# Kernel tuning notes

Hardware: AMD Instinct MI355X
Metric: run time of the kernel (lower is better)

## Reference

```python
import jax, jax.numpy as jnp
import numpy as np

N_NODES = 50000
EPS_BN = 1e-5

def _gat_layer(x, W, a_src, a_dst, b, src, dst):
    # PyG GATConv: h = xW per head; e = LeakyReLU(a_src.h_j + a_dst.h_i);
    # softmax over incoming edges per destination; out_i = sum alpha_e * h_j.
    N = x.shape[0]
    H, C = a_src.shape
    h = (x @ W).reshape(N, H, C)                       # [N,H,C]
    s = jnp.sum(h * a_src[None], axis=-1)              # [N,H] source term
    d = jnp.sum(h * a_dst[None], axis=-1)              # [N,H] dest term
    e = jax.nn.leaky_relu(s[src] + d[dst], 0.2)        # [E,H]
    m = jax.ops.segment_max(e, dst, num_segments=N)
    m = jnp.where(jnp.isfinite(m), m, 0.0)             # isolated nodes
    ex = jnp.exp(e - m[dst])                           # [E,H]
    denom = jax.ops.segment_sum(ex, dst, num_segments=N)
    alpha = ex / (denom[dst] + 1e-16)                  # [E,H]
    out = jax.ops.segment_sum(alpha[:, :, None] * h[src], dst, num_segments=N)
    return out.reshape(N, H * C) + b

def _bn_eval(x, gamma, beta, mean, var):
    return (x - mean) * jax.lax.rsqrt(var + EPS_BN) * gamma + beta

def setup_inputs() -> dict:
    key = jax.random.key(0)
    ks = jax.random.split(key, 12)
    N, E, Fin, H = N_NODES, 800000, 128, 4
    C1, C2 = 64, 32
    x = jax.random.normal(ks[0], (N, Fin), jnp.float32)
    edge_index = jax.random.randint(ks[1], (2, E), 0, N, jnp.int64)
    sc = lambda f: 1.0 / np.sqrt(f)
    return {
        "x": x, "edge_index": edge_index,
        "W1": jax.random.normal(ks[2], (Fin, H * C1), jnp.float32) * sc(Fin),
        "a1_src": jax.random.normal(ks[3], (H, C1), jnp.float32) * sc(C1),
        "a1_dst": jax.random.normal(ks[4], (H, C1), jnp.float32) * sc(C1),
        "b1": jnp.zeros((H * C1,), jnp.float32),
        "g1": jnp.ones((H * C1,), jnp.float32),
        "be1": jnp.zeros((H * C1,), jnp.float32),
        "m1": jnp.zeros((H * C1,), jnp.float32),
        "v1": jnp.ones((H * C1,), jnp.float32),
        "W2": jax.random.normal(ks[5], (H * C1, H * C2), jnp.float32) * sc(H * C1),
        "a2_src": jax.random.normal(ks[6], (H, C2), jnp.float32) * sc(C2),
        "a2_dst": jax.random.normal(ks[7], (H, C2), jnp.float32) * sc(C2),
        "b2": jnp.zeros((H * C2,), jnp.float32),
        "g2": jnp.ones((H * C2,), jnp.float32),
        "be2": jnp.zeros((H * C2,), jnp.float32),
        "m2": jnp.zeros((H * C2,), jnp.float32),
        "v2": jnp.ones((H * C2,), jnp.float32),
        "fcW": jax.random.normal(ks[8], (H * C2, 1), jnp.float32) * sc(H * C2),
        "fcb": jnp.zeros((1,), jnp.float32),
    }

def reference(x, edge_index, W1, a1_src, a1_dst, b1, g1, be1, m1, v1,
              W2, a2_src, a2_dst, b2, g2, be2, m2, v2, fcW, fcb):
    N = x.shape[0]
    loops = jnp.arange(N, dtype=edge_index.dtype)
    src = jnp.concatenate([edge_index[0], loops])  # PyG adds self-loops
    dst = jnp.concatenate([edge_index[1], loops])
    h = _gat_layer(x, W1, a1_src, a1_dst, b1, src, dst)
    h = jax.nn.elu(_bn_eval(h, g1, be1, m1, v1))
    h = _gat_layer(h, W2, a2_src, a2_dst, b2, src, dst)
    h = jax.nn.elu(_bn_eval(h, g2, be2, m2, v2))
    return h @ fcW + fcb
```

## Files before the change

kernel.cpp:

```cpp
#include <hip/hip_runtime.h>
#include <hip/hip_bf16.h>

#define NN 50000
#define EE 800000
#define ETOT 850000
#define FIN 128
#define HC1 256
#define HC2 128
#define CAP 64
#define NB 196
#define CAPC 5632
#define SOFTMAX_M 20.0f
#define NT1 17
#define NT2 9
#define L2E 1.4426950408889634f

typedef __hip_bfloat16 bf16;
typedef unsigned short u16;
typedef unsigned int u32;
typedef unsigned long long u64;
typedef __attribute__((ext_vector_type(8))) short short8;
typedef __attribute__((ext_vector_type(4))) float f32x4;
typedef __attribute__((ext_vector_type(8))) unsigned short us8;

__device__ __forceinline__ float b2f(bf16 v) { return __bfloat162float(v); }
__device__ __forceinline__ float bu2f(u16 v) { return __uint_as_float(((u32)v) << 16); }
__device__ __forceinline__ float blo(u32 v) { return __uint_as_float(v << 16); }
__device__ __forceinline__ float bhi(u32 v) { return __uint_as_float(v & 0xffff0000u); }
__device__ __forceinline__ u16 f2bu(float f) { return __bfloat16_as_ushort(__float2bfloat16(f)); }
__device__ __forceinline__ float ldf(const void* p, int flag, int i) {
    return flag ? bu2f(((const u16*)p)[i]) : ((const float*)p)[i];
}
__device__ __forceinline__ float elu(float o) {
    return (o > 0.f) ? o : exp2f(o * L2E) - 1.f;
}

__device__ __forceinline__ int detect_f(const void* p, int nelem) {
    int lane = threadIdx.x & 63;
    int m = nelem < 64 ? nelem : 64;
    u16 v = (lane < m) ? ((const u16*)p)[lane] : (u16)0;
    int ex = (v >> 7) & 0xFF;
    u64 nzm   = __ballot(v != 0);
    u64 sanem = __ballot(v != 0 && ex >= 96 && ex <= 143);
    u64 oddm  = __ballot(v != 0 && (lane & 1));
    u64 evenm = __ballot(v != 0 && !(lane & 1));
    int c_nz = __popcll(nzm);
    if (c_nz == 0) return 1;
    if (__popcll(evenm) == 0 && __popcll(oddm) > 0) return 0;
    return (__popcll(sanem) * 10 >= c_nz * 9) ? 1 : 0;
}

__device__ __forceinline__ int detect_ei(const int* w) {
    int lane = threadIdx.x & 63;
    int v = w[lane];
    u64 oddm  = __ballot(v != 0 && (lane & 1));
    u64 evenm = __ballot(v != 0 && !(lane & 1));
    return (__popcll(oddm) == 0 && __popcll(evenm) > 0) ? 1 : 0;
}

struct Ptrs { const void* p[20]; };

__device__ const int g_small_map[18]  = {2,10,3,4,5,6,7,8,9,11,12,13,14,15,16,17,18,19};
__device__ const int g_small_n[18]    = {32768,32768,256,256,256,256,256,256,256,128,128,128,128,128,128,128,128,1};
__device__ const int g_small_off[18]  = {0,32768,65536,65792,66048,66304,66560,66816,67072,
                                         67328,67456,67584,67712,67840,67968,68096,68224,68352};

__global__ __launch_bounds__(256) void k_prepA(Ptrs ptrs, float* __restrict__ SM,
                                               u16* __restrict__ Wt1, u16* __restrict__ Wt2,
                                               int* __restrict__ gfill, u32* __restrict__ coarse) {
    __shared__ int hist[NB], basev[NB], cursor[NB];
    int b = blockIdx.x, tid = threadIdx.x;
    if (b < 18) {
        int t = g_small_map[b];
        int n = g_small_n[b];
        float* dst = SM + g_small_off[b];
        const void* src = ptrs.p[t];
        int f = detect_f(src, n);
        for (int i = tid; i < n; i += 256) dst[i] = ldf(src, f, i);
    } else if (b < 146) {
        int k = b - 18;
        const void* W = ptrs.p[2];
        int fW = detect_f(W, 32768);
        int fs = detect_f(ptrs.p[3], 256);
        int fd = detect_f(ptrs.p[4], 256);
        for (int n = tid; n < NT1 * 16; n += 256) {
            float w = 0.f;
            if (n < HC1) w = ldf(W, fW, k * HC1 + n);
            else if (n < HC1 + 8) {
                int c8 = n - HC1, hd = c8 & 3, isd = c8 >> 2;
                const void* a = isd ? ptrs.p[4] : ptrs.p[3];
                int fa = isd ? fd : fs;
                float acc = 0.f;
                for (int c = 0; c < 64; c++)
                    acc += ldf(W, fW, k * HC1 + hd * 64 + c) * ldf(a, fa, hd * 64 + c);
                w = acc;
            }
            int kt = k >> 5, q = (k >> 3) & 3, j = k & 7, nt = n >> 4, nl = n & 15;
            Wt1[((kt * NT1 + nt) * 16 + nl) * 32 + q * 8 + j] = f2bu(w);
        }
    } else if (b < 402) {
        int k = b - 146;
        const void* W = ptrs.p[10];
        int fW = detect_f(W, 32768);
        int fs = detect_f(ptrs.p[11], 128);
        int fd = detect_f(ptrs.p[12], 128);
        for (int n = tid; n < NT2 * 16; n += 256) {
            float w = 0.f;
            if (n < HC2) w = ldf(W, fW, k * HC2 + n);
            else if (n < HC2 + 8) {
                int c8 = n - HC2, hd = c8 & 3, isd = c8 >> 2;
                const void* a = isd ? ptrs.p[12] : ptrs.p[11];
                int fa = isd ? fd : fs;
                float acc = 0.f;
                for (int c = 0; c < 32; c++)
                    acc += ldf(W, fW, k * HC2 + hd * 32 + c) * ldf(a, fa, hd * 32 + c);
                w = acc;
            }
            int kt = k >> 5, q = (k >> 3) & 3, j = k & 7, nt = n >> 4, nl = n & 15;
            Wt2[((kt * NT2 + nt) * 16 + nl) * 32 + q * 8 + j] = f2bu(w);
        }
    } else {
        int p = b - 402;
        const int* ei = (const int*)ptrs.p[1];
        int f = detect_ei(ei);
        for (int i = tid; i < NB; i += 256) { hist[i] = 0; cursor[i] = 0; }
        __syncthreads();
        u32 pe[16];
#pragma unroll
        for (int j = 0; j < 16; j++) {
            int e = p * 4096 + j * 256 + tid;
            if (e < ETOT) {
                int sn, dn;
                if (e < EE) {
                    if (f) { sn = ei[2 * e]; dn = ei[2 * (EE + e)]; }
                    else   { sn = ei[e];     dn = ei[EE + e]; }
                } else { sn = e - EE; dn = sn; }
                pe[j] = ((u32)dn << 16) | (u32)sn;
                atomicAdd(&hist[dn >> 8], 1);
            } else pe[j] = 0xFFFFFFFFu;
        }
        __syncthreads();
        for (int i = tid; i < NB; i += 256) basev[i] = atomicAdd(&gfill[i], hist[i]);
        __syncthreads();
#pragma unroll
        for (int j = 0; j < 16; j++) {
            if (pe[j] != 0xFFFFFFFFu) {
                int bin = pe[j] >> 24;
                int off = basev[bin] + atomicAdd(&cursor[bin], 1);
                if (off < CAPC) coarse[(size_t)bin * CAPC + off] = pe[j];
            }
        }
    }
}

__global__ __launch_bounds__(256) void k_prepB(Ptrs ptrs, const int* __restrict__ gfill,
                                               const u32* __restrict__ coarse,
                                               int* __restrict__ fill, u16* __restrict__ col16,
                                               const u16* __restrict__ Wt,
                                               u16* __restrict__ h, float* __restrict__ s, float* __restrict__ d,
                                               const float* __restrict__ SM, float* __restrict__ CSB) {
    __shared__ int h2[256], cur2[256];
    int b = blockIdx.x, tid = threadIdx.x;
    if (b < NB) {
        int nbase = b * 256;
        int cnt_b = min(gfill[b], CAPC);
        h2[tid] = 0; cur2[tid] = 0;
        __syncthreads();
        for (int i = tid; i < cnt_b; i += 256)
            atomicAdd(&h2[(coarse[(size_t)b * CAPC + i] >> 16) & 255], 1);
        __syncthreads();
        int n = nbase + tid;
        if (n < NN) fill[n] = h2[tid];
        for (int i = tid; i < cnt_b; i += 256) {
            u32 pe = coarse[(size_t)b * CAPC + i];
            int dl = (pe >> 16) & 255;
            int slot = atomicAdd(&cur2[dl], 1);
            if (slot < CAP) col16[(size_t)(nbase + dl) * CAP + slot] = (u16)(pe & 0xFFFFu);
        }
        return;
    }
    if (b == NB) {
        if (tid < 256) {
            float rs = rsqrtf(SM[67072 + tid] + 1e-5f);
            float cs = SM[66304 + tid] * rs;
            CSB[tid] = cs;
            CSB[256 + tid] = (SM[66048 + tid] - SM[66816 + tid]) * cs + SM[66560 + tid];
            if (tid < 128) {
                float rs2 = rsqrtf(SM[68096 + tid] + 1e-5f);
                float cs2 = SM[67712 + tid] * rs2;
                CSB[512 + tid] = cs2;
                CSB[640 + tid] = (SM[67584 + tid] - SM[67968 + tid]) * cs2 + SM[67840 + tid];
            }
        }
        return;
    }
    const void* xraw = ptrs.p[0];
    int f = detect_f(xraw, NN * FIN);
    int w = (b - NB - 1) * 4 + (tid >> 6);
    if (w >= NN / 16) return;
    int lane = tid & 63;
    int nl = lane & 15, q = lane >> 4;
    short8 a[4];
    if (f) {
        const u16* ap = (const u16*)xraw + (size_t)(w * 16 + nl) * FIN;
#pragma unroll
        for (int kt = 0; kt < 4; kt++) a[kt] = *(const short8*)&ap[kt * 32 + q * 8];
    } else {
        const float* ap = (const float*)xraw + (size_t)(w * 16 + nl) * FIN;
#pragma unroll
        for (int kt = 0; kt < 4; kt++) {
            float4 x0 = *(const float4*)&ap[kt * 32 + q * 8];
            float4 x1 = *(const float4*)&ap[kt * 32 + q * 8 + 4];
            short8 v;
            v[0] = (short)f2bu(x0.x); v[1] = (short)f2bu(x0.y);
            v[2] = (short)f2bu(x0.z); v[3] = (short)f2bu(x0.w);
            v[4] = (short)f2bu(x1.x); v[5] = (short)f2bu(x1.y);
            v[6] = (short)f2bu(x1.z); v[7] = (short)f2bu(x1.w);
            a[kt] = v;
        }
    }
#pragma unroll
    for (int nt = 0; nt < NT1; nt++) {
        f32x4 acc = {0.f, 0.f, 0.f, 0.f};
        const u16* bp = Wt + (size_t)(nt * 16 + nl) * 32 + q * 8;
        acc = __builtin_amdgcn_mfma_f32_16x16x32_bf16(a[0], *(const short8*)&bp[(0 * NT1) * 512], acc, 0, 0, 0);
        acc = __builtin_amdgcn_mfma_f32_16x16x32_bf16(a[1], *(const short8*)&bp[(1 * NT1) * 512], acc, 0, 0, 0);
        acc = __builtin_amdgcn_mfma_f32_16x16x32_bf16(a[2], *(const short8*)&bp[(2 * NT1) * 512], acc, 0, 0, 0);
        acc = __builtin_amdgcn_mfma_f32_16x16x32_bf16(a[3], *(const short8*)&bp[(3 * NT1) * 512], acc, 0, 0, 0);
        if (nt < 16) {
            int colx = nt * 16 + nl;
#pragma unroll
            for (int r = 0; r < 4; r++)
                h[(size_t)(w * 16 + q * 4 + r) * HC1 + colx] = f2bu(acc[r]);
        } else if (nl < 8) {
#pragma unroll
            for (int r = 0; r < 4; r++) {
                int row = w * 16 + q * 4 + r;
                if (nl < 4) s[row * 4 + nl] = acc[r];
                else        d[row * 4 + (nl - 4)] = acc[r];
            }
        }
    }
}

__global__ __launch_bounds__(256) void k_mm2(const u16* __restrict__ xb, const u16* __restrict__ Wt,
                                             u16* __restrict__ h, float* __restrict__ s, float* __restrict__ d) {
    int w = blockIdx.x * 4 + (threadIdx.x >> 6);
    if (w >= NN / 16) return;
    int lane = threadIdx.x & 63;
    int nl = lane & 15, q = lane >> 4;
    const u16* ap = xb + (size_t)(w * 16 + nl) * HC1;
    short8 a[8];
#pragma unroll
    for (int kt = 0; kt < 8; kt++) a[kt] = *(const short8*)&ap[kt * 32 + q * 8];
#pragma unroll
    for (int nt = 0; nt < NT2; nt++) {
        f32x4 acc = {0.f, 0.f, 0.f, 0.f};
        const u16* bp = Wt + (size_t)(nt * 16 + nl) * 32 + q * 8;
#pragma unroll
        for (int kt = 0; kt < 8; kt++)
            acc = __builtin_amdgcn_mfma_f32_16x16x32_bf16(a[kt], *(const short8*)&bp[(kt * NT2) * 512], acc, 0, 0, 0);
        if (nt < 8) {
            int colx = nt * 16 + nl;
#pragma unroll
            for (int r = 0; r < 4; r++)
                h[(size_t)(w * 16 + q * 4 + r) * HC2 + colx] = f2bu(acc[r]);
        } else if (nl < 8) {
#pragma unroll
            for (int r = 0; r < 4; r++) {
                int row = w * 16 + q * 4 + r;
                if (nl < 4) s[row * 4 + nl] = acc[r];
                else        d[row * 4 + (nl - 4)] = acc[r];
            }
        }
    }
}

__global__ __launch_bounds__(256) void k_node1(const int* __restrict__ fill, const u16* __restrict__ col16,
                                               const float* __restrict__ sterm, const float* __restrict__ dterm,
                                               const u16* __restrict__ h,
                                               const float* __restrict__ CS, const float* __restrict__ CB,
                                               u16* __restrict__ outb) {
    int wid = __builtin_amdgcn_readfirstlane(threadIdx.x >> 6);
    int lane = threadIdx.x & 63;
    int half = lane >> 5;
    int l5 = lane & 31;
    int n = blockIdx.x * 4 + wid;
    int hd = l5 >> 3;
    int c0 = l5 * 8;
    int cnt = min(fill[n], CAP);
    float dn = dterm[n * 4 + hd];
    const float WO = SOFTMAX_M * L2E;
    int allidx = (int)col16[(size_t)n * CAP + lane];
    float den = 0.f;
    float acc[8];
#pragma unroll
    for (int k = 0; k < 8; k++) acc[k] = 0.f;
    const u16* hb = h + c0;
    if (cnt > 0) {
        int C = (cnt + 7) >> 3;
        float svA[4], svB[4]; uint4 qA[4], qB[4];
#pragma unroll
        for (int p = 0; p < 4; p++) {
            int e = 2 * p + half;
            int idx = __shfl(allidx, (e < cnt) ? e : 0);
            idx = ((unsigned)idx < NN) ? idx : 0;
            svA[p] = sterm[idx * 4 + hd];
            qA[p] = *(const uint4*)(hb + (size_t)idx * HC1);
        }
        int c = 0;
        while (true) {
            if (c + 1 < C) {
#pragma unroll
                for (int p = 0; p < 4; p++) {
                    int e = (c + 1) * 8 + 2 * p + half;
                    int idx = __shfl(allidx, (e < cnt) ? e : 0);
                    idx = ((unsigned)idx < NN) ? idx : 0;
                    svB[p] = sterm[idx * 4 + hd];
                    qB[p] = *(const uint4*)(hb + (size_t)idx * HC1);
                }
            }
#pragma unroll
            for (int p = 0; p < 4; p++) {
                int e = c * 8 + 2 * p + half;
                float t = svA[p] + dn;
                float lr = fmaxf(t, 0.2f * t);
                float w = exp2f(fmaf(lr, L2E, -WO));
                w = (e < cnt) ? w : 0.f;
                den += w;
                acc[0] = fmaf(w, blo(qA[p].x), acc[0]); acc[1] = fmaf(w, bhi(qA[p].x), acc[1]);
                acc[2] = fmaf(w, blo(qA[p].y), acc[2]); acc[3] = fmaf(w, bhi(qA[p].y), acc[3]);
                acc[4] = fmaf(w, blo(qA[p].z), acc[4]); acc[5] = fmaf(w, bhi(qA[p].z), acc[5]);
                acc[6] = fmaf(w, blo(qA[p].w), acc[6]); acc[7] = fmaf(w, bhi(qA[p].w), acc[7]);
            }
            c++;
            if (c >= C) break;
#pragma unroll
            for (int p = 0; p < 4; p++) { svA[p] = svB[p]; qA[p] = qB[p]; }
        }
    }
    den += __shfl_xor(den, 32);
#pragma unroll
    for (int k = 0; k < 8; k++) acc[k] += __shfl_xor(acc[k], 32);
    float inv = 1.f / (den + 1e-16f);
    float4 cs0 = *(const float4*)&CS[c0], cs1 = *(const float4*)&CS[c0 + 4];
    float4 cb0 = *(const float4*)&CB[c0], cb1 = *(const float4*)&CB[c0 + 4];
    float csa[8] = {cs0.x, cs0.y, cs0.z, cs0.w, cs1.x, cs1.y, cs1.z, cs1.w};
    float cba[8] = {cb0.x, cb0.y, cb0.z, cb0.w, cb1.x, cb1.y, cb1.z, cb1.w};
    us8 ov;
#pragma unroll
    for (int k = 0; k < 8; k++) {
        float o = fmaf(acc[k] * inv, csa[k], cba[k]);
        ov[k] = f2bu(elu(o));
    }
    if (half == 0)
        *(us8*)&outb[(size_t)n * HC1 + c0] = ov;
}

__global__ __launch_bounds__(256) void k_node2fc(const int* __restrict__ fill, const u16* __restrict__ col16,
                                                 const float* __restrict__ sterm, const float* __restrict__ dterm,
                                                 const u16* __restrict__ h,
                                                 const float* __restrict__ CS, const float* __restrict__ CB,
                                                 const float* __restrict__ fcw, const float* __restrict__ fcb,
                                                 float* __restrict__ out) {
    int wid = __builtin_amdgcn_readfirstlane(threadIdx.x >> 6);
    int lane = threadIdx.x & 63;
    int half = lane >> 5;
    int l5 = lane & 31;
    int n = blockIdx.x * 4 + wid;
    int hd = l5 >> 3;
    int c0 = l5 * 4;
    int cnt = min(fill[n], CAP);
    float dn = dterm[n * 4 + hd];
    const float WO = SOFTMAX_M * L2E;
    int allidx = (int)col16[(size_t)n * CAP + lane];
    float den = 0.f;
    float acc[4] = {0.f, 0.f, 0.f, 0.f};
    const u16* hb = h + c0;
    if (cnt > 0) {
        int C = (cnt + 7) >> 3;
        float svA[4], svB[4]; uint2 qA[4], qB[4];
#pragma unroll
        for (int p = 0; p < 4; p++) {
            int e = 2 * p + half;
            int idx = __shfl(allidx, (e < cnt) ? e : 0);
            idx = ((unsigned)idx < NN) ? idx : 0;
            svA[p] = sterm[idx * 4 + hd];
            qA[p] = *(const uint2*)(hb + (size_t)idx * HC2);
        }
        int c = 0;
        while (true) {
            if (c + 1 < C) {
#pragma unroll
                for (int p = 0; p < 4; p++) {
                    int e = (c + 1) * 8 + 2 * p + half;
                    int idx = __shfl(allidx, (e < cnt) ? e : 0);
                    idx = ((unsigned)idx < NN) ? idx : 0;
                    svB[p] = sterm[idx * 4 + hd];
                    qB[p] = *(const uint2*)(hb + (size_t)idx * HC2);
                }
            }
#pragma unroll
            for (int p = 0; p < 4; p++) {
                int e = c * 8 + 2 * p + half;
                float t = svA[p] + dn;
                float lr = fmaxf(t, 0.2f * t);
                float w = exp2f(fmaf(lr, L2E, -WO));
                w = (e < cnt) ? w : 0.f;
                den += w;
                acc[0] = fmaf(w, blo(qA[p].x), acc[0]); acc[1] = fmaf(w, bhi(qA[p].x), acc[1]);
                acc[2] = fmaf(w, blo(qA[p].y), acc[2]); acc[3] = fmaf(w, bhi(qA[p].y), acc[3]);
            }
            c++;
            if (c >= C) break;
#pragma unroll
            for (int p = 0; p < 4; p++) { svA[p] = svB[p]; qA[p] = qB[p]; }
        }
    }
    den += __shfl_xor(den, 32);
#pragma unroll
    for (int k = 0; k < 4; k++) acc[k] += __shfl_xor(acc[k], 32);
    float inv = 1.f / (den + 1e-16f);
    float4 cs = *(const float4*)&CS[c0];
    float4 cb = *(const float4*)&CB[c0];
    float o0 = elu(fmaf(acc[0] * inv, cs.x, cb.x));
    float o1 = elu(fmaf(acc[1] * inv, cs.y, cb.y));
    float o2 = elu(fmaf(acc[2] * inv, cs.z, cb.z));
    float o3 = elu(fmaf(acc[3] * inv, cs.w, cb.w));
    float4 fw = *(const float4*)&fcw[c0];
    float v = o0 * fw.x + o1 * fw.y + o2 * fw.z + o3 * fw.w;
    if (half) v = 0.f;
#pragma unroll
    for (int o = 32; o > 0; o >>= 1) v += __shfl_xor(v, o);
    if (lane == 0) out[n] = v + fcb[0];
}

extern "C" void kernel_launch(void* const* d_in, const int* in_sizes, int n_in,
                              void* d_out, int out_size, void* d_ws, size_t ws_size,
                              hipStream_t stream) {
    float* out = (float*)d_out;

    char* wsb = (char*)d_ws;
    size_t off = 0;
    auto alloc = [&](size_t bytes) -> void* {
        void* p = wsb + off;
        off += (bytes + 255) & ~(size_t)255;
        return p;
    };
    float* SM     = (float*)alloc((size_t)68353 * sizeof(float));
    float* CSB    = (float*)alloc((size_t)768 * sizeof(float));
    u16*   Wt1    = (u16*)alloc((size_t)4 * NT1 * 512 * sizeof(u16));
    u16*   Wt2    = (u16*)alloc((size_t)8 * NT2 * 512 * sizeof(u16));
    int*   gfill  = (int*)alloc(NB * sizeof(int));
    u32*   coarse = (u32*)alloc((size_t)NB * CAPC * sizeof(u32));
    int*   fill   = (int*)alloc(NN * sizeof(int));
    u16*   col16  = (u16*)alloc((size_t)NN * CAP * sizeof(u16));
    float* s1     = (float*)alloc((size_t)NN * 4 * sizeof(float));
    float* d1     = (float*)alloc((size_t)NN * 4 * sizeof(float));
    float* s2     = (float*)alloc((size_t)NN * 4 * sizeof(float));
    float* d2     = (float*)alloc((size_t)NN * 4 * sizeof(float));
    u16*   h1     = (u16*)alloc((size_t)NN * HC1 * sizeof(u16));
    u16*   hb1    = (u16*)alloc((size_t)NN * HC1 * sizeof(u16));
    u16*   h2     = (u16*)alloc((size_t)NN * HC2 * sizeof(u16));

    float* FCW = SM + 68224;
    float* FCB = SM + 68352;
    float* CS1 = CSB;
    float* CB1 = CSB + 256;
    float* CS2 = CSB + 512;
    float* CB2 = CSB + 640;

    Ptrs ptrs;
    for (int i = 0; i < 20; i++) ptrs.p[i] = d_in[i];

    int gW  = (NN / 16 + 3) / 4;
    int gA  = 402 + 208;
    int gB  = NB + 1 + gW;

    hipMemsetAsync(gfill, 0, NB * sizeof(int), stream);

    k_prepA<<<gA, 256, 0, stream>>>(ptrs, SM, Wt1, Wt2, gfill, coarse);
    k_prepB<<<gB, 256, 0, stream>>>(ptrs, gfill, coarse, fill, col16, Wt1, h1, s1, d1, SM, CSB);
    k_node1<<<NN / 4, 256, 0, stream>>>(fill, col16, s1, d1, h1, CS1, CB1, hb1);
    k_mm2<<<gW, 256, 0, stream>>>(hb1, Wt2, h2, s2, d2);
    k_node2fc<<<NN / 4, 256, 0, stream>>>(fill, col16, s2, d2, h2, CS2, CB2, FCW, FCB, out);
}
```

Baseline: 200.4 us.

## Slice layer-1 features into 32-column planes and gather per slice

The first GEMM now writes h1 as eight column-slice planes of 32 bf16 values per node instead of row-major 256-wide rows. The layer-1 aggregation kernel launches eight times as many blocks, each handling one slice, so a wave gathers 64-byte rows from a 3.2 MB plane. This is meant to give the random neighbor gathers better cache locality. In exchange the per-edge index, s-term and exp work is repeated for each slice, and cross-lane reductions are added.

```diff
diff --git a/kernel.cpp b/kernel.cpp
--- a/kernel.cpp
+++ b/kernel.cpp
@@ -229,9 +229,10 @@
         acc = __builtin_amdgcn_mfma_f32_16x16x32_bf16(a[3], *(const short8*)&bp[(3 * NT1) * 512], acc, 0, 0, 0);
         if (nt < 16) {
             int colx = nt * 16 + nl;
+            int sl = colx >> 5, cc = colx & 31;
 #pragma unroll
             for (int r = 0; r < 4; r++)
-                h[(size_t)(w * 16 + q * 4 + r) * HC1 + colx] = f2bu(acc[r]);
+                h[((size_t)sl * NN + (w * 16 + q * 4 + r)) * 32 + cc] = f2bu(acc[r]);
         } else if (nl < 8) {
 #pragma unroll
             for (int r = 0; r < 4; r++) {
@@ -278,83 +279,69 @@
 
 __global__ __launch_bounds__(256) void k_node1(const int* __restrict__ fill, const u16* __restrict__ col16,
                                                const float* __restrict__ sterm, const float* __restrict__ dterm,
-                                               const u16* __restrict__ h,
+                                               const u16* __restrict__ hs,
                                                const float* __restrict__ CS, const float* __restrict__ CB,
                                                u16* __restrict__ outb) {
+    int bid = blockIdx.x;
+    int sl = bid & 7;
     int wid = __builtin_amdgcn_readfirstlane(threadIdx.x >> 6);
+    int n = (bid >> 3) * 4 + wid;
+    if (n >= NN) return;
     int lane = threadIdx.x & 63;
-    int half = lane >> 5;
-    int l5 = lane & 31;
-    int n = blockIdx.x * 4 + wid;
-    int hd = l5 >> 3;
-    int c0 = l5 * 8;
+    int g = lane >> 3;
+    int j = lane & 7;
+    int hd = sl >> 1;
     int cnt = min(fill[n], CAP);
     float dn = dterm[n * 4 + hd];
     const float WO = SOFTMAX_M * L2E;
     int allidx = (int)col16[(size_t)n * CAP + lane];
+    const u16* hsl = hs + (size_t)sl * NN * 32 + j * 4;
     float den = 0.f;
-    float acc[8];
-#pragma unroll
-    for (int k = 0; k < 8; k++) acc[k] = 0.f;
-    const u16* hb = h + c0;
-    if (cnt > 0) {
-        int C = (cnt + 7) >> 3;
-        float svA[4], svB[4]; uint4 qA[4], qB[4];
-#pragma unroll
-        for (int p = 0; p < 4; p++) {
-            int e = 2 * p + half;
-            int idx = __shfl(allidx, (e < cnt) ? e : 0);
-            idx = ((unsigned)idx < NN) ? idx : 0;
-            svA[p] = sterm[idx * 4 + hd];
-            qA[p] = *(const uint4*)(hb + (size_t)idx * HC1);
-        }
-        int c = 0;
-        while (true) {
-            if (c + 1 < C) {
-#pragma unroll
-                for (int p = 0; p < 4; p++) {
-                    int e = (c + 1) * 8 + 2 * p + half;
-                    int idx = __shfl(allidx, (e < cnt) ? e : 0);
-                    idx = ((unsigned)idx < NN) ? idx : 0;
-                    svB[p] = sterm[idx * 4 + hd];
-                    qB[p] = *(const uint4*)(hb + (size_t)idx * HC1);
-                }
-            }
-#pragma unroll
-            for (int p = 0; p < 4; p++) {
-                int e = c * 8 + 2 * p + half;
-                float t = svA[p] + dn;
-                float lr = fmaxf(t, 0.2f * t);
-                float w = exp2f(fmaf(lr, L2E, -WO));
-                w = (e < cnt) ? w : 0.f;
-                den += w;
-                acc[0] = fmaf(w, blo(qA[p].x), acc[0]); acc[1] = fmaf(w, bhi(qA[p].x), acc[1]);
-                acc[2] = fmaf(w, blo(qA[p].y), acc[2]); acc[3] = fmaf(w, bhi(qA[p].y), acc[3]);
-                acc[4] = fmaf(w, blo(qA[p].z), acc[4]); acc[5] = fmaf(w, bhi(qA[p].z), acc[5]);
-                acc[6] = fmaf(w, blo(qA[p].w), acc[6]); acc[7] = fmaf(w, bhi(qA[p].w), acc[7]);
-            }
-            c++;
-            if (c >= C) break;
-#pragma unroll
-            for (int p = 0; p < 4; p++) { svA[p] = svB[p]; qA[p] = qB[p]; }
-        }
-    }
-    den += __shfl_xor(den, 32);
-#pragma unroll
-    for (int k = 0; k < 8; k++) acc[k] += __shfl_xor(acc[k], 32);
+    float a0 = 0.f, a1 = 0.f, a2 = 0.f, a3 = 0.f;
+    int C = (cnt + 15) >> 4;
+    for (int c = 0; c < C; c++) {
+        int e0 = c * 16 + g;
+        int e1 = e0 + 8;
+        int i0 = __shfl(allidx, (e0 < cnt) ? e0 : 0);
+        int i1 = __shfl(allidx, (e1 < cnt) ? e1 : 0);
+        i0 = ((unsigned)i0 < NN) ? i0 : 0;
+        i1 = ((unsigned)i1 < NN) ? i1 : 0;
+        float sv0 = sterm[i0 * 4 + hd];
+        float sv1 = sterm[i1 * 4 + hd];
+        uint2 q0 = *(const uint2*)(hsl + (size_t)i0 * 32);
+        uint2 q1 = *(const uint2*)(hsl + (size_t)i1 * 32);
+        float t0 = sv0 + dn, t1 = sv1 + dn;
+        float lr0 = fmaxf(t0, 0.2f * t0), lr1 = fmaxf(t1, 0.2f * t1);
+        float w0 = exp2f(fmaf(lr0, L2E, -WO));
+        float w1 = exp2f(fmaf(lr1, L2E, -WO));
+        w0 = (e0 < cnt) ? w0 : 0.f;
+        w1 = (e1 < cnt) ? w1 : 0.f;
+        den += w0 + w1;
+        a0 = fmaf(w0, blo(q0.x), a0); a1 = fmaf(w0, bhi(q0.x), a1);
+        a2 = fmaf(w0, blo(q0.y), a2); a3 = fmaf(w0, bhi(q0.y), a3);
+        a0 = fmaf(w1, blo(q1.x), a0); a1 = fmaf(w1, bhi(q1.x), a1);
+        a2 = fmaf(w1, blo(q1.y), a2); a3 = fmaf(w1, bhi(q1.y), a3);
+    }
+#pragma unroll
+    for (int m = 8; m <= 32; m <<= 1) {
+        den += __shfl_xor(den, m);
+        a0 += __shfl_xor(a0, m); a1 += __shfl_xor(a1, m);
+        a2 += __shfl_xor(a2, m); a3 += __shfl_xor(a3, m);
+    }
     float inv = 1.f / (den + 1e-16f);
-    float4 cs0 = *(const float4*)&CS[c0], cs1 = *(const float4*)&CS[c0 + 4];
-    float4 cb0 = *(const float4*)&CB[c0], cb1 = *(const float4*)&CB[c0 + 4];
-    float csa[8] = {cs0.x, cs0.y, cs0.z, cs0.w, cs1.x, cs1.y, cs1.z, cs1.w};
-    float cba[8] = {cb0.x, cb0.y, cb0.z, cb0.w, cb1.x, cb1.y, cb1.z, cb1.w};
-    us8 ov;
-#pragma unroll
-    for (int k = 0; k < 8; k++) {
-        float o = fmaf(acc[k] * inv, csa[k], cba[k]);
-        ov[k] = f2bu(elu(o));
-    }
-    if (half == 0)
-        *(us8*)&outb[(size_t)n * HC1 + c0] = ov;
+    int c0 = sl * 32 + j * 4;
+    float4 cs = *(const float4*)&CS[c0];
+    float4 cb = *(const float4*)&CB[c0];
+    float o0 = elu(fmaf(a0 * inv, cs.x, cb.x));
+    float o1 = elu(fmaf(a1 * inv, cs.y, cb.y));
+    float o2 = elu(fmaf(a2 * inv, cs.z, cb.z));
+    float o3 = elu(fmaf(a3 * inv, cs.w, cb.w));
+    if (g == 0) {
+        uint2 pk;
+        pk.x = ((u32)f2bu(o0)) | (((u32)f2bu(o1)) << 16);
+        pk.y = ((u32)f2bu(o2)) | (((u32)f2bu(o3)) << 16);
+        *(uint2*)&outb[(size_t)n * HC1 + c0] = pk;
+    }
 }
 
 __global__ __launch_bounds__(256) void k_node2fc(const int* __restrict__ fill, const u16* __restrict__ col16,
@@ -476,12 +463,13 @@
     int gW  = (NN / 16 + 3) / 4;
     int gA  = 402 + 208;
     int gB  = NB + 1 + gW;
+    int gN1 = 8 * (NN / 4);
 
     hipMemsetAsync(gfill, 0, NB * sizeof(int), stream);
 
     k_prepA<<<gA, 256, 0, stream>>>(ptrs, SM, Wt1, Wt2, gfill, coarse);
     k_prepB<<<gB, 256, 0, stream>>>(ptrs, gfill, coarse, fill, col16, Wt1, h1, s1, d1, SM, CSB);
-    k_node1<<<NN / 4, 256, 0, stream>>>(fill, col16, s1, d1, h1, CS1, CB1, hb1);
+    k_node1<<<gN1, 256, 0, stream>>>(fill, col16, s1, d1, h1, CS1, CB1, hb1);
     k_mm2<<<gW, 256, 0, stream>>>(hb1, Wt2, h2, s2, d2);
     k_node2fc<<<NN / 4, 256, 0, stream>>>(fill, col16, s2, d2, h2, CS2, CB2, FCW, FCB, out);
 }
```

Result: slower. 274.0 us (+36.7%).
